# Performance work log

Measured on AMD Instinct MI355X. Metric: run time of the kernel, lower is better.

Reference implementation:

```python
import jax, jax.numpy as jnp
import numpy as np

EMBED = 1024
HEADS = 16
HEAD_DIM = EMBED // HEADS


def setup_inputs() -> dict:
    key = jax.random.key(0)
    ks = jax.random.split(key, 9)
    s = 1.0 / np.sqrt(EMBED)
    return {
        "embeddings": jax.random.normal(ks[0], (4, 2048, EMBED), dtype=jnp.float32),
        "wq": jax.random.uniform(ks[1], (EMBED, EMBED), jnp.float32, -s, s),
        "bq": jax.random.uniform(ks[2], (EMBED,), jnp.float32, -s, s),
        "wk": jax.random.uniform(ks[3], (EMBED, EMBED), jnp.float32, -s, s),
        "bk": jax.random.uniform(ks[4], (EMBED,), jnp.float32, -s, s),
        "wv": jax.random.uniform(ks[5], (EMBED, EMBED), jnp.float32, -s, s),
        "bv": jax.random.uniform(ks[6], (EMBED,), jnp.float32, -s, s),
        "wo": jax.random.uniform(ks[7], (EMBED, EMBED), jnp.float32, -s, s),
        "bo": jax.random.uniform(ks[8], (EMBED,), jnp.float32, -s, s),
    }


def reference(embeddings, wq, bq, wk, bk, wv, bv, wo, bo):
    b, s, _ = embeddings.shape
    # Projections: x @ W^T + b (torch nn.Linear convention)
    q = (embeddings @ wq.T + bq).reshape(b, s, HEADS, HEAD_DIM)
    k = (embeddings @ wk.T + bk).reshape(b, s, HEADS, HEAD_DIM)
    v = (embeddings @ wv.T + bv).reshape(b, s, HEADS, HEAD_DIM)
    scale = 1.0 / np.sqrt(HEAD_DIM).astype(np.float32)
    # scores: [b, h, s, s]
    scores = jnp.einsum("bqhd,bkhd->bhqk", q, k) * scale
    probs = jax.nn.softmax(scores, axis=-1)
    attn = jnp.einsum("bhqk,bkhd->bqhd", probs, v).reshape(b, s, EMBED)
    return attn @ wo.T + bo
```

## Files before the change

### kernel.cpp

```cpp
#include <hip/hip_runtime.h>
#include <hip/hip_bf16.h>
#include <math.h>

using bf16x8 = __attribute__((ext_vector_type(8))) short;
using f32x4  = __attribute__((ext_vector_type(4))) float;
using f32x16 = __attribute__((ext_vector_type(16))) float;
using i32x4  = __attribute__((ext_vector_type(4))) int;
using i32x2  = __attribute__((ext_vector_type(2))) int;

#define MFMA_BF16(a, b, c) __builtin_amdgcn_mfma_f32_16x16x32_bf16((a), (b), (c), 0, 0, 0)
#define MFMA32(a, b, c)    __builtin_amdgcn_mfma_f32_32x32x16_bf16((a), (b), (c), 0, 0, 0)

__device__ __forceinline__ float bf2f(short s) {
    union { unsigned u; float f; } v;
    v.u = ((unsigned)(unsigned short)s) << 16;
    return v.f;
}
__device__ __forceinline__ short f2bf(float f) {
    union { float f; unsigned u; } v; v.f = f;
    unsigned r = v.u + 0x7FFF + ((v.u >> 16) & 1);
    return (short)(r >> 16);
}
__device__ __forceinline__ int cvtpk_bf16(float lo, float hi) {
    int r;
    asm("v_cvt_pk_bf16_f32 %0, %1, %2" : "=v"(r) : "v"(lo), "v"(hi));
    return r;
}
__device__ __forceinline__ void permswap(int &a, int &b) {
#if __has_builtin(__builtin_amdgcn_permlane32_swap)
    typedef unsigned u32x2v __attribute__((ext_vector_type(2)));
    u32x2v r = __builtin_amdgcn_permlane32_swap((unsigned)a, (unsigned)b, false, false);
    a = (int)r[0]; b = (int)r[1];
#else
    asm volatile("v_permlane32_swap_b32 %0, %1" : "+v"(a), "+v"(b));
#endif
}
__device__ __forceinline__ float fexp2(float x) {
#if __has_builtin(__builtin_amdgcn_exp2f)
    return __builtin_amdgcn_exp2f(x);
#else
    return exp2f(x);
#endif
}

__device__ __forceinline__ void gload_lds16(const void* g, void* l) {
    __builtin_amdgcn_global_load_lds(
        (const __attribute__((address_space(1))) void*)g,
        (__attribute__((address_space(3))) void*)l, 16, 0, 0);
}

__global__ void detect_dtype(const unsigned short* __restrict__ emb, int* flag) {
    __shared__ int tot;
    if (threadIdx.x == 0) tot = 0;
    __syncthreads();
    int c = 0;
    for (int i = 0; i < 64; i++) {
        unsigned short v = emb[2 * (threadIdx.x * 64 + i)];
        unsigned e = (v >> 7) & 0xFF;
        if (v == 0 || v == 0x8000u || (e >= 97 && e <= 137)) c++;
    }
    atomicAdd(&tot, c);
    __syncthreads();
    if (threadIdx.x == 0) *flag = (tot > 8192) ? 1 : 0;
}

__global__ void convert8(const void* __restrict__ src, short* __restrict__ dst,
                         int n8, const int* __restrict__ flag) {
    int i = blockIdx.x * 256 + threadIdx.x;
    if (i >= n8) return;
    if (*flag) {
        ((bf16x8*)dst)[i] = ((const bf16x8*)src)[i];
    } else {
        const float* f = (const float*)src + (size_t)i * 8;
        bf16x8 o;
#pragma unroll
        for (int j = 0; j < 8; j++) o[j] = f2bf(f[j]);
        ((bf16x8*)dst)[i] = o;
    }
}

__global__ void convert_all(
    const void* __restrict__ w0, const void* __restrict__ w1,
    const void* __restrict__ w2, const void* __restrict__ w3,
    const void* __restrict__ b0, const void* __restrict__ b1,
    const void* __restrict__ b2, const void* __restrict__ b3,
    short* dw0, short* dw1, short* dw2, short* dw3,
    short* db0, short* db1, short* db2, short* db3,
    const int* __restrict__ flag)
{
    int i = blockIdx.x * 256 + threadIdx.x;
    const void* src; short* dst; int idx;
    if (i < 524288) {
        int w = i >> 17; idx = i & 131071;
        src = (w == 0) ? w0 : (w == 1) ? w1 : (w == 2) ? w2 : w3;
        dst = (w == 0) ? dw0 : (w == 1) ? dw1 : (w == 2) ? dw2 : dw3;
    } else {
        int j = i - 524288; int b = j >> 7; idx = j & 127;
        src = (b == 0) ? b0 : (b == 1) ? b1 : (b == 2) ? b2 : b3;
        dst = (b == 0) ? db0 : (b == 1) ? db1 : (b == 2) ? db2 : db3;
    }
    if (*flag) {
        ((bf16x8*)dst)[idx] = ((const bf16x8*)src)[idx];
    } else {
        const float* f = (const float*)src + (size_t)idx * 8;
        bf16x8 o;
#pragma unroll
        for (int j = 0; j < 8; j++) o[j] = f2bf(f[j]);
        ((bf16x8*)dst)[idx] = o;
    }
}

__global__ __launch_bounds__(256) void gemm128(
    const short* __restrict__ A,
    const short* __restrict__ B0, const short* __restrict__ B1,
    const short* __restrict__ B2,
    const short* __restrict__ bias0, const short* __restrict__ bias1,
    const short* __restrict__ bias2,
    void* __restrict__ C0, void* __restrict__ C1, void* __restrict__ C2,
    float s0, float s1, float s2,
    int mode0, int mode1, int mode2,
    const int* __restrict__ flag)
{
    constexpr int M = 8192, N = 1024, Kd = 1024, BK = 32;
    __shared__ __align__(16) short As[2][128 * BK];
    __shared__ __align__(16) short Bs[2][128 * BK];

    const int z = blockIdx.z;
    const short* B    = (z == 0) ? B0    : (z == 1) ? B1    : B2;
    const short* bias = (z == 0) ? bias0 : (z == 1) ? bias1 : bias2;
    void*  C     = (z == 0) ? C0 : (z == 1) ? C1 : C2;
    float  scale = (z == 0) ? s0 : (z == 1) ? s1 : s2;
    int    mode  = (z == 0) ? mode0 : (z == 1) ? mode1 : mode2;

    const int tid  = threadIdx.x;
    const int lane = tid & 63;
    const int wave = tid >> 6;
    const int lr   = lane & 15;
    const int quad = lane >> 4;

    const int bid = blockIdx.x;
    const int swz = ((bid & 7) << 6) | (bid >> 3);
    const int m0 = (swz >> 3) * 128;
    const int n0 = (swz & 7) * 128;
    const int wm = (wave >> 1) * 64;
    const int wn = (wave & 1) * 64;

    const int srow = lane >> 2;
    const int scol = (((lane & 3) ^ ((lane >> 3) & 3)) * 8);
    const int rchunk = (quad ^ ((lr >> 1) & 3)) * 8;

    int fl = 1;
    if (mode == 2) fl = *flag;

    f32x4 acc[4][4];
#pragma unroll
    for (int i = 0; i < 4; i++)
#pragma unroll
        for (int j = 0; j < 4; j++) acc[i][j] = (f32x4){0.f, 0.f, 0.f, 0.f};

    auto stage = [&](int bufi, int k) {
#pragma unroll
        for (int t = 0; t < 2; t++) {
            const int r = wave * 32 + t * 16;
            gload_lds16(A + (size_t)(m0 + r + srow) * Kd + k + scol,
                        &As[bufi][r * BK]);
            gload_lds16(B + (size_t)(n0 + r + srow) * Kd + k + scol,
                        &Bs[bufi][r * BK]);
        }
    };

    stage(0, 0);
    for (int k0 = 0; k0 < Kd; k0 += BK) {
        const int cur = (k0 >> 5) & 1;
        stage(cur ^ 1, (k0 + BK) & (Kd - 1));
        asm volatile("s_waitcnt vmcnt(4)" ::: "memory");
        __builtin_amdgcn_s_barrier();
        __builtin_amdgcn_sched_barrier(0);

        bf16x8 a[4], b[4];
#pragma unroll
        for (int i = 0; i < 4; i++)
            a[i] = *(const bf16x8*)(&As[cur][(wm + i * 16 + lr) * BK + rchunk]);
#pragma unroll
        for (int j = 0; j < 4; j++)
            b[j] = *(const bf16x8*)(&Bs[cur][(wn + j * 16 + lr) * BK + rchunk]);
#pragma unroll
        for (int i = 0; i < 4; i++)
#pragma unroll
            for (int j = 0; j < 4; j++)
                acc[i][j] = MFMA_BF16(a[i], b[j], acc[i][j]);

        asm volatile("s_waitcnt lgkmcnt(0)" ::: "memory");
        __builtin_amdgcn_sched_barrier(0);
        __builtin_amdgcn_s_barrier();
    }

    if (mode == 1) {
#pragma unroll
        for (int j = 0; j < 4; j++) {
            const int col = n0 + wn + j * 16 + lr;
            const float bv = bf2f(bias[col]);
#pragma unroll
            for (int i = 0; i < 4; i++) {
                const int row = m0 + wm + i * 16 + quad * 4;
                const float v0 = (acc[i][j][0] + bv) * scale;
                const float v1 = (acc[i][j][1] + bv) * scale;
                const float v2 = (acc[i][j][2] + bv) * scale;
                const float v3 = (acc[i][j][3] + bv) * scale;
                i32x2 dd;
                dd[0] = cvtpk_bf16(v0, v1);
                dd[1] = cvtpk_bf16(v2, v3);
                *(i32x2*)((short*)C + (size_t)col * M + row) = dd;
            }
        }
    } else {
#pragma unroll
        for (int j = 0; j < 4; j++) {
            const int col = n0 + wn + j * 16 + lr;
            const float bv = bf2f(bias[col]);
#pragma unroll
            for (int i = 0; i < 4; i++) {
#pragma unroll
                for (int r = 0; r < 4; r++) {
                    const int row = m0 + wm + i * 16 + quad * 4 + r;
                    const float v = (acc[i][j][r] + bv) * scale;
                    if (mode == 0) ((short*)C)[(size_t)row * N + col] = f2bf(v);
                    else {
                        if (fl) ((short*)C)[(size_t)row * N + col] = f2bf(v);
                        else    ((float*)C)[(size_t)row * N + col] = v;
                    }
                }
            }
        }
    }
}

__global__ __launch_bounds__(256) void attn_kernel(
    const short* Q, const short* __restrict__ K,
    const short* __restrict__ Vt, short* Aout)
{
    __shared__ __align__(16) short lds[2][2][64][64];

    const int tid  = threadIdx.x;
    const int lane = tid & 63;
    const int wave = tid >> 6;
    const int l31  = lane & 31;
    const int hi   = lane >> 5;
    const int xr   = (l31 & 7) ^ ((l31 >> 3) & 3);

    const int qt = blockIdx.x;
    const int bh = blockIdx.y;
    const int b  = bh >> 4, h = bh & 15;
    const int q0 = b * 2048 + qt * 128 + wave * 32;
    const int c0 = h * 64;

    const int sr  = lane >> 3;
    const int scb = (lane & 7) ^ sr;
    const int sarr = wave >> 1;

    const short* Kb = K  + (size_t)(b * 2048) * 1024 + c0;
    const short* Vb = Vt + (size_t)c0 * 8192 + b * 2048;

    bf16x8 qf[4];
#pragma unroll
    for (int slot = 0; slot < 4; slot++)
        qf[slot] = *(const bf16x8*)(Q + (size_t)(q0 + l31) * 1024 + c0 + slot * 16 + hi * 8);

    auto stage = [&](int bufi, int kt) {
#pragma unroll
        for (int t = 0; t < 4; t++) {
            const int r0 = ((wave & 1) * 4 + t) * 8;
            const int sc = (scb ^ t) * 8;
            short* dst = &lds[bufi][sarr][r0][0];
            if (sarr == 0)
                gload_lds16(Kb + (size_t)(kt + r0 + sr) * 1024 + sc, dst);
            else
                gload_lds16(Vb + (size_t)(r0 + sr) * 8192 + kt + sc, dst);
        }
    };

    bf16x8 onesf;
#pragma unroll
    for (int j = 0; j < 8; j++) onesf[j] = (short)0x3F80;

    f32x16 o[2], l_acc;
#pragma unroll
    for (int r = 0; r < 16; r++) { o[0][r] = 0.f; o[1][r] = 0.f; l_acc[r] = 0.f; }

    stage(0, 0);
    for (int kt = 0; kt < 2048; kt += 64) {
        const int cur = (kt >> 6) & 1;
        stage(cur ^ 1, (kt + 64) & 2047);
        asm volatile("s_waitcnt vmcnt(4)" ::: "memory");
        __builtin_amdgcn_s_barrier();
        __builtin_amdgcn_sched_barrier(0);

        f32x16 st[2];
#pragma unroll
        for (int blk = 0; blk < 2; blk++) {
#pragma unroll
            for (int r = 0; r < 16; r++) st[blk][r] = 0.f;
#pragma unroll
            for (int slot = 0; slot < 4; slot++) {
                bf16x8 kf = *(const bf16x8*)
                    &lds[cur][0][blk * 32 + l31][(((slot << 1) | hi) ^ xr) * 8];
                st[blk] = MFMA32(kf, qf[slot], st[blk]);
            }
        }

#pragma unroll
        for (int blk = 0; blk < 2; blk++)
#pragma unroll
            for (int r = 0; r < 16; r++)
                st[blk][r] = fexp2(st[blk][r]);

#pragma unroll
        for (int ks = 0; ks < 4; ks++) {
            const int blk = ks >> 1;
            const int rb  = (ks & 1) * 8;
            int A0 = cvtpk_bf16(st[blk][rb + 0], st[blk][rb + 1]);
            int A1 = cvtpk_bf16(st[blk][rb + 2], st[blk][rb + 3]);
            int B0 = cvtpk_bf16(st[blk][rb + 4], st[blk][rb + 5]);
            int B1 = cvtpk_bf16(st[blk][rb + 6], st[blk][rb + 7]);
            permswap(A0, B0);
            permswap(A1, B1);
            i32x4 paw; paw[0] = A0; paw[1] = A1; paw[2] = B0; paw[3] = B1;
            const bf16x8 pf = *(const bf16x8*)&paw;
            l_acc = MFMA32(pf, onesf, l_acc);
#pragma unroll
            for (int dblk = 0; dblk < 2; dblk++) {
                bf16x8 vf = *(const bf16x8*)
                    &lds[cur][1][dblk * 32 + l31][(((ks << 1) | hi) ^ xr) * 8];
                o[dblk] = MFMA32(pf, vf, o[dblk]);
            }
        }

        asm volatile("s_waitcnt lgkmcnt(0)" ::: "memory");
        __builtin_amdgcn_sched_barrier(0);
        __builtin_amdgcn_s_barrier();
    }

#pragma unroll
    for (int r = 0; r < 16; r++) {
        const int qrow = (r & 3) + 8 * (r >> 2) + 4 * hi;
        const float inv = 1.f / l_acc[r];
#pragma unroll
        for (int dblk = 0; dblk < 2; dblk++)
            Aout[(size_t)(q0 + qrow) * 1024 + c0 + dblk * 32 + l31] =
                f2bf(o[dblk][r] * inv);
    }
}

extern "C" void kernel_launch(void* const* d_in, const int* in_sizes, int n_in,
                              void* d_out, int out_size, void* d_ws, size_t ws_size,
                              hipStream_t stream)
{
    const size_t MB = (size_t)1024 * 1024;
    char* ws = (char*)d_ws;

    int*   flagp = (int*)ws;
    short* embC  = (short*)(ws + 1 * MB);
    short* wC[4] = { (short*)(ws + 17 * MB), (short*)(ws + 19 * MB),
                     (short*)(ws + 21 * MB), (short*)(ws + 23 * MB) };
    short* bC[4] = { (short*)(ws + 25 * MB), (short*)(ws + 25 * MB + 4096),
                     (short*)(ws + 25 * MB + 8192), (short*)(ws + 25 * MB + 12288) };

    short *Qb, *Kb, *Vt, *Ab;
    if (ws_size >= 90 * MB) {
        Qb = (short*)(ws + 26 * MB);
        Kb = (short*)(ws + 42 * MB);
        Vt = (short*)(ws + 58 * MB);
        Ab = (short*)(ws + 74 * MB);
    } else {
        Qb = (short*)(ws + 26 * MB);
        Kb = (short*)d_out;
        Vt = (short*)(ws + 42 * MB);
        Ab = Qb;
    }

    detect_dtype<<<1, 256, 0, stream>>>((const unsigned short*)d_in[0], flagp);

    convert8<<<4096, 256, 0, stream>>>(d_in[0], embC, 1048576, flagp);
    convert_all<<<2050, 256, 0, stream>>>(
        d_in[1], d_in[3], d_in[5], d_in[7],
        d_in[2], d_in[4], d_in[6], d_in[8],
        wC[0], wC[1], wC[2], wC[3],
        bC[0], bC[1], bC[2], bC[3], flagp);

    dim3 blk(256);
    gemm128<<<dim3(512, 1, 3), blk, 0, stream>>>(
        embC, wC[0], wC[1], wC[2], bC[0], bC[1], bC[2],
        Qb, Kb, Vt, 0.18033688011112042f, 1.0f, 1.0f, 0, 0, 1, nullptr);

    attn_kernel<<<dim3(16, 64), blk, 0, stream>>>(Qb, Kb, Vt, Ab);

    gemm128<<<dim3(512, 1, 1), blk, 0, stream>>>(
        Ab, wC[3], nullptr, nullptr, bC[3], nullptr, nullptr,
        d_out, nullptr, nullptr, 1.0f, 0.f, 0.f, 2, 0, 0, flagp);
}
```

Measured before the change: 311.6 us.

## Switch projection GEMM to 32x32x16 MFMA with triple-buffered LDS pipeline

The projection GEMM now uses 32x32x16 bf16 MFMA tiles instead of 16x16x32, with a new LDS swizzle and fragment indexing plus a matching epilogue layout. The LDS staging goes from double to triple buffering, prefetching two k-steps ahead with a looser vmcnt wait. The larger MFMA shape is meant to cut LDS fragment reads per FLOP, and the deeper prefetch to hide global load latency. In exchange, LDS use per block rises and the epilogue's store pattern becomes more strided.

Measured after the change: 333.6 us. +7.0%, slower.

```diff
diff --git a/kernel.cpp b/kernel.cpp
--- a/kernel.cpp
+++ b/kernel.cpp
@@ -122,8 +122,8 @@
     const int* __restrict__ flag)
 {
     constexpr int M = 8192, N = 1024, Kd = 1024, BK = 32;
-    __shared__ __align__(16) short As[2][128 * BK];
-    __shared__ __align__(16) short Bs[2][128 * BK];
+    __shared__ __align__(16) short As[3][128 * BK];
+    __shared__ __align__(16) short Bs[3][128 * BK];
 
     const int z = blockIdx.z;
     const short* B    = (z == 0) ? B0    : (z == 1) ? B1    : B2;
@@ -135,8 +135,8 @@
     const int tid  = threadIdx.x;
     const int lane = tid & 63;
     const int wave = tid >> 6;
-    const int lr   = lane & 15;
-    const int quad = lane >> 4;
+    const int l31  = lane & 31;
+    const int hi   = lane >> 5;
 
     const int bid = blockIdx.x;
     const int swz = ((bid & 7) << 6) | (bid >> 3);
@@ -146,17 +146,19 @@
     const int wn = (wave & 1) * 64;
 
     const int srow = lane >> 2;
-    const int scol = (((lane & 3) ^ ((lane >> 3) & 3)) * 8);
-    const int rchunk = (quad ^ ((lr >> 1) & 3)) * 8;
+    const int scol = ((lane & 3) ^ ((lane >> 2) & 3)) * 8;
+    const int xr = l31 & 3;
 
     int fl = 1;
     if (mode == 2) fl = *flag;
 
-    f32x4 acc[4][4];
-#pragma unroll
-    for (int i = 0; i < 4; i++)
-#pragma unroll
-        for (int j = 0; j < 4; j++) acc[i][j] = (f32x4){0.f, 0.f, 0.f, 0.f};
+    f32x16 acc[2][2];
+#pragma unroll
+    for (int i = 0; i < 2; i++)
+#pragma unroll
+        for (int j = 0; j < 2; j++)
+#pragma unroll
+            for (int r = 0; r < 16; r++) acc[i][j][r] = 0.f;
 
     auto stage = [&](int bufi, int k) {
 #pragma unroll
@@ -170,59 +172,70 @@
     };
 
     stage(0, 0);
+    stage(1, BK);
+    int cur = 0, pre = 2;
     for (int k0 = 0; k0 < Kd; k0 += BK) {
-        const int cur = (k0 >> 5) & 1;
-        stage(cur ^ 1, (k0 + BK) & (Kd - 1));
-        asm volatile("s_waitcnt vmcnt(4)" ::: "memory");
+        stage(pre, (k0 + 2 * BK) & (Kd - 1));
+        asm volatile("s_waitcnt vmcnt(8)" ::: "memory");
         __builtin_amdgcn_s_barrier();
         __builtin_amdgcn_sched_barrier(0);
 
-        bf16x8 a[4], b[4];
-#pragma unroll
-        for (int i = 0; i < 4; i++)
-            a[i] = *(const bf16x8*)(&As[cur][(wm + i * 16 + lr) * BK + rchunk]);
-#pragma unroll
-        for (int j = 0; j < 4; j++)
-            b[j] = *(const bf16x8*)(&Bs[cur][(wn + j * 16 + lr) * BK + rchunk]);
-#pragma unroll
-        for (int i = 0; i < 4; i++)
-#pragma unroll
-            for (int j = 0; j < 4; j++)
-                acc[i][j] = MFMA_BF16(a[i], b[j], acc[i][j]);
+        bf16x8 a[2][2], b[2][2];
+#pragma unroll
+        for (int i = 0; i < 2; i++)
+#pragma unroll
+            for (int s = 0; s < 2; s++) {
+                a[i][s] = *(const bf16x8*)
+                    (&As[cur][(wm + i * 32 + l31) * BK + (((s << 1) | hi) ^ xr) * 8]);
+                b[i][s] = *(const bf16x8*)
+                    (&Bs[cur][(wn + i * 32 + l31) * BK + (((s << 1) | hi) ^ xr) * 8]);
+            }
+#pragma unroll
+        for (int s = 0; s < 2; s++)
+#pragma unroll
+            for (int i = 0; i < 2; i++)
+#pragma unroll
+                for (int j = 0; j < 2; j++)
+                    acc[i][j] = MFMA32(a[i][s], b[j][s], acc[i][j]);
 
         asm volatile("s_waitcnt lgkmcnt(0)" ::: "memory");
         __builtin_amdgcn_sched_barrier(0);
         __builtin_amdgcn_s_barrier();
+        cur = (cur == 2) ? 0 : cur + 1;
+        pre = (pre == 2) ? 0 : pre + 1;
     }
 
     if (mode == 1) {
 #pragma unroll
-        for (int j = 0; j < 4; j++) {
-            const int col = n0 + wn + j * 16 + lr;
+        for (int j = 0; j < 2; j++) {
+            const int col = n0 + wn + j * 32 + l31;
             const float bv = bf2f(bias[col]);
 #pragma unroll
-            for (int i = 0; i < 4; i++) {
-                const int row = m0 + wm + i * 16 + quad * 4;
-                const float v0 = (acc[i][j][0] + bv) * scale;
-                const float v1 = (acc[i][j][1] + bv) * scale;
-                const float v2 = (acc[i][j][2] + bv) * scale;
-                const float v3 = (acc[i][j][3] + bv) * scale;
-                i32x2 dd;
-                dd[0] = cvtpk_bf16(v0, v1);
-                dd[1] = cvtpk_bf16(v2, v3);
-                *(i32x2*)((short*)C + (size_t)col * M + row) = dd;
+            for (int i = 0; i < 2; i++) {
+#pragma unroll
+                for (int g = 0; g < 4; g++) {
+                    const int row = m0 + wm + i * 32 + g * 8 + 4 * hi;
+                    const float v0 = (acc[i][j][g * 4 + 0] + bv) * scale;
+                    const float v1 = (acc[i][j][g * 4 + 1] + bv) * scale;
+                    const float v2 = (acc[i][j][g * 4 + 2] + bv) * scale;
+                    const float v3 = (acc[i][j][g * 4 + 3] + bv) * scale;
+                    i32x2 dd;
+                    dd[0] = cvtpk_bf16(v0, v1);
+                    dd[1] = cvtpk_bf16(v2, v3);
+                    *(i32x2*)((short*)C + (size_t)col * M + row) = dd;
+                }
             }
         }
     } else {
 #pragma unroll
-        for (int j = 0; j < 4; j++) {
-            const int col = n0 + wn + j * 16 + lr;
+        for (int j = 0; j < 2; j++) {
+            const int col = n0 + wn + j * 32 + l31;
             const float bv = bf2f(bias[col]);
 #pragma unroll
-            for (int i = 0; i < 4; i++) {
-#pragma unroll
-                for (int r = 0; r < 4; r++) {
-                    const int row = m0 + wm + i * 16 + quad * 4 + r;
+            for (int i = 0; i < 2; i++) {
+#pragma unroll
+                for (int r = 0; r < 16; r++) {
+                    const int row = m0 + wm + i * 32 + (r & 3) + 8 * (r >> 2) + 4 * hi;
                     const float v = (acc[i][j][r] + bv) * scale;
                     if (mode == 0) ((short*)C)[(size_t)row * N + col] = f2bf(v);
                     else {
```
